# Kernel optimization log

Hardware: AMD Instinct MI355X
Metric: run time of the kernel (lower is better)

## Reference

```python
import jax, jax.numpy as jnp
import numpy as np

T_IN, A_IN, V_IN = 300, 74, 36
T_H, A_H, V_H = 256, 64, 64
ATTN_IN = 2 * (T_H + A_H + V_H)   # 768
MEM = 256
NN1 = NN2 = G1D = G2D = 512
OUT_IN = T_H + A_H + V_H + MEM    # 640
OUT_H, OUT_D = 512, 1
T_STEPS, N = 128, 512


def setup_inputs() -> dict:
    key = jax.random.key(0)
    ks = iter(jax.random.split(key, 64))

    def w(shape):
        return (jax.random.normal(next(ks), shape, jnp.float32) * 0.05)

    inp = {
        "x_p": jax.random.normal(next(ks), (T_STEPS, N, T_IN + A_IN + V_IN), jnp.float32),
        "c_t": jnp.zeros((N, T_H), jnp.float32),
        "c_a": jnp.zeros((N, A_H), jnp.float32),
        "c_v": jnp.zeros((N, V_H), jnp.float32),
        "mem": jnp.zeros((N, MEM), jnp.float32),
        # LSTMCell params (PyTorch layout: W_ih [4H, in], W_hh [4H, H], fused bias)
        "t_Wi": w((4 * T_H, T_IN)), "t_Wh": w((4 * T_H, T_H)), "t_b": w((4 * T_H,)),
        "a_Wi": w((4 * A_H, A_IN)), "a_Wh": w((4 * A_H, A_H)), "a_b": w((4 * A_H,)),
        "v_Wi": w((4 * V_H, V_IN)), "v_Wh": w((4 * V_H, V_H)), "v_b": w((4 * V_H,)),
        # attention / gating MLPs (PyTorch Linear layout: [out, in])
        "attn1_w1": w((NN1, ATTN_IN)), "attn1_b1": w((NN1,)),
        "attn1_w2": w((ATTN_IN, NN1)), "attn1_b2": w((ATTN_IN,)),
        "attn2_w1": w((NN2, ATTN_IN)), "attn2_b1": w((NN2,)),
        "attn2_w2": w((MEM, NN2)), "attn2_b2": w((MEM,)),
        "g1_w1": w((G1D, ATTN_IN + MEM)), "g1_b1": w((G1D,)),
        "g1_w2": w((MEM, G1D)), "g1_b2": w((MEM,)),
        "g2_w1": w((G2D, ATTN_IN + MEM)), "g2_b1": w((G2D,)),
        "g2_w2": w((MEM, G2D)), "g2_b2": w((MEM,)),
        "out_w1": w((OUT_H, OUT_IN)), "out_b1": w((OUT_H,)),
        "out_w2": w((OUT_D, OUT_H)), "out_b2": w((OUT_D,)),
    }
    return inp


def _lstm_cell(x, h, c, Wi, Wh, b):
    # PyTorch LSTMCell: gates ordered i, f, g, o
    z = x @ Wi.T + h @ Wh.T + b
    i, f, g, o = jnp.split(z, 4, axis=1)
    c2 = jax.nn.sigmoid(f) * c + jax.nn.sigmoid(i) * jnp.tanh(g)
    h2 = jax.nn.sigmoid(o) * jnp.tanh(c2)
    return h2, c2


def _mlp2(x, w1, b1, w2, b2):
    return jax.nn.relu(x @ w1.T + b1) @ w2.T + b2


def reference(x_p, c_t, c_a, c_v, mem,
              t_Wi, t_Wh, t_b, a_Wi, a_Wh, a_b, v_Wi, v_Wh, v_b,
              attn1_w1, attn1_b1, attn1_w2, attn1_b2,
              attn2_w1, attn2_b1, attn2_w2, attn2_b2,
              g1_w1, g1_b1, g1_w2, g1_b2,
              g2_w1, g2_b1, g2_w2, g2_b2,
              out_w1, out_b1, out_w2, out_b2):
    n = x_p.shape[1]
    init = (jnp.zeros((n, T_H), x_p.dtype), c_t,
            jnp.zeros((n, A_H), x_p.dtype), c_a,
            jnp.zeros((n, V_H), x_p.dtype), c_v,
            mem)

    def step(carry, x):
        th, tc, ah, ac, vh, vc, m = carry
        xt = x[:, :T_IN]
        xa = x[:, T_IN:T_IN + A_IN]
        xv = x[:, T_IN + A_IN:]
        pre_c = jnp.concatenate([tc, ac, vc], axis=1)
        th2, tc2 = _lstm_cell(xt, th, tc, t_Wi, t_Wh, t_b)
        ah2, ac2 = _lstm_cell(xa, ah, ac, a_Wi, a_Wh, a_b)
        vh2, vc2 = _lstm_cell(xv, vh, vc, v_Wi, v_Wh, v_b)
        cur_c = jnp.concatenate([tc2, ac2, vc2], axis=1)
        c_star = jnp.concatenate([pre_c, cur_c], axis=1)          # [n, 768]
        attention = jax.nn.softmax(_mlp2(c_star, attn1_w1, attn1_b1, attn1_w2, attn1_b2), axis=1)
        attended = attention * c_star
        c_hat = jnp.tanh(_mlp2(attended, attn2_w1, attn2_b1, attn2_w2, attn2_b2))
        both = jnp.concatenate([attended, m], axis=1)             # [n, 1024]
        gamma1 = jax.nn.sigmoid(_mlp2(both, g1_w1, g1_b1, g1_w2, g1_b2))
        gamma2 = jax.nn.sigmoid(_mlp2(both, g2_w1, g2_b1, g2_w2, g2_b2))
        m2 = gamma1 * m + gamma2 * c_hat
        return (th2, tc2, ah2, ac2, vh2, vc2, m2), None

    (th, tc, ah, ac, vh, vc, m), _ = jax.lax.scan(step, init, x_p)
    last_h = jnp.concatenate([th, ah, vh, m], axis=1)             # [n, 640]
    return _mlp2(last_h, out_w1, out_b1, out_w2, out_b2)          # [n, 1]
```

## Files before the change

kernel.cpp:

```cpp
#include <hip/hip_runtime.h>
#include <hip/hip_bf16.h>
#include <hip/hip_fp16.h>

typedef unsigned int u32;
typedef unsigned long long u64;
typedef __fp16 h2t __attribute__((ext_vector_type(2)));

#define T_STEPS_D 128
#define NBATCH 512

#define OFF_TWI   0L
#define OFF_AWI   284672L
#define OFF_VWI   302592L
#define OFF_A1W1  315392L
#define OFF_A1W2  512000L
#define OFF_A2W1  708608L
#define OFF_A2W2  905216L
#define OFF_GW1   970752L
#define OFF_GW2   1495040L
#define OFF_OW1   1626112L
#define U32_TOTAL 1789952L
#define FLAGS_OFF 1791744L
#define ATTQ_OFF  1792000L
#define OWP_OFF   2578432L
#define ATOMIC_RLX_AG(p, v) __hip_atomic_store((p), (v), __ATOMIC_RELAXED, __HIP_MEMORY_SCOPE_AGENT)
#define ATOMIC_LD_AG(p)     __hip_atomic_load((p), __ATOMIC_RELAXED, __HIP_MEMORY_SCOPE_AGENT)

__device__ __forceinline__ float sigm(float x) { return 1.f / (1.f + __expf(-x)); }
__device__ __forceinline__ float tanh_fast(float x) {
    float e = __expf(2.f * x);
    return 1.f - 2.f / (e + 1.f);
}
__device__ __forceinline__ float dot2(u32 a, u32 b, float c) {
    union { u32 u; h2t h; } x, y; x.u = a; y.u = b;
#if __has_builtin(__builtin_amdgcn_fdot2)
    return __builtin_amdgcn_fdot2(x.h, y.h, c, false);
#else
    c += (float)x.h[0] * (float)y.h[0];
    c += (float)x.h[1] * (float)y.h[1];
    return c;
#endif
}
__device__ __forceinline__ u32 pk2(float a, float b) {
    union { h2t h; u32 u; } z;
    z.h = __builtin_amdgcn_cvt_pkrtz(a, b);
    return z.u;
}

__device__ __forceinline__ void gp_load1(u32* buf, const u32* __restrict__ wp, int N) {
#pragma unroll
    for (int q = 0; q < 4; ++q) {
        uint2 v = *(const uint2*)(wp + q * 2 * N);
        buf[2 * q] = v.x; buf[2 * q + 1] = v.y;
    }
}
__device__ __forceinline__ void gp_load2(u32* buf, const u32* __restrict__ wp, int N) {
#pragma unroll
    for (int q = 0; q < 4; ++q) {
        uint4 v = *(const uint4*)(wp + q * 2 * N);
        buf[4 * q] = v.x; buf[4 * q + 1] = v.y; buf[4 * q + 2] = v.z; buf[4 * q + 3] = v.w;
    }
}

template<int NC>
__device__ __forceinline__ void gp_comp(float* acc, const u32* __restrict__ a, int stA,
                                        int kb, const u32* buf) {
#pragma unroll
    for (int r = 0; r < 4; ++r) {
        uint4 xa = *(const uint4*)(a + r * stA + kb);
        uint4 xb = *(const uint4*)(a + r * stA + kb + 4);
        u32 av[8] = {xa.x, xa.y, xa.z, xa.w, xb.x, xb.y, xb.z, xb.w};
#pragma unroll
        for (int p = 0; p < 8; ++p) {
            if constexpr (NC == 1) {
                acc[r] = dot2(buf[p], av[p], acc[r]);
            } else {
                acc[2 * r]     = dot2(buf[4 * (p >> 1) + (p & 1)],     av[p], acc[2 * r]);
                acc[2 * r + 1] = dot2(buf[4 * (p >> 1) + 2 + (p & 1)], av[p], acc[2 * r + 1]);
            }
        }
    }
}

template<int NC, int DEPTH>
__device__ __forceinline__ void gpart(float* acc, const u32* __restrict__ a, int k2, int stA,
                                      const u32* __restrict__ w, int N)
{
    const int nb = k2 >> 3;
    u32 b0[NC * 8], b1[NC * 8], b2[NC * 8];
#define GLOAD(B, P) do { if constexpr (NC == 1) gp_load1(B, w + (long)(P) * 8 * N, N); \
                         else gp_load2(B, w + (long)(P) * 8 * N, N); } while (0)
    if (nb > 0) GLOAD(b0, 0);
    if (DEPTH > 1 && nb > 1) GLOAD(b1, 1);
    if (DEPTH > 2 && nb > 2) GLOAD(b2, 2);
    int i = 0;
    while (i < nb) {
        gp_comp<NC>(acc, a, stA, i * 8, b0);
        if (i + DEPTH < nb) GLOAD(b0, i + DEPTH);
        ++i; if (i >= nb) break;
        gp_comp<NC>(acc, a, stA, i * 8, b1);
        if (i + DEPTH < nb) GLOAD(b1, i + DEPTH);
        ++i; if (i >= nb) break;
        if (DEPTH > 2) {
            gp_comp<NC>(acc, a, stA, i * 8, b2);
            if (i + DEPTH < nb) GLOAD(b2, i + DEPTH);
            ++i;
        }
    }
#undef GLOAD
    for (int p = nb * 8; p < k2; ++p) {
        const u32* wp = w + (long)(p >> 1) * 2 * N + (p & 1);
#pragma unroll
        for (int r = 0; r < 4; ++r) {
            u32 aa = a[r * stA + p];
            if constexpr (NC == 1) {
                acc[r] = dot2(wp[0], aa, acc[r]);
            } else {
                acc[2 * r]     = dot2(wp[0], aa, acc[2 * r]);
                acc[2 * r + 1] = dot2(wp[2], aa, acc[2 * r + 1]);
            }
        }
    }
}

__global__ void k_transpose(const float* __restrict__ src, unsigned short* __restrict__ dst,
                            int N, int K, int strideU, int rowOffK, int colOff)
{
    long i = (long)blockIdx.x * 256 + threadIdx.x;
    if (i >= (long)N * K) return;
    int n = (int)(i / K);
    int k = (int)(i - (long)n * K);
    __half h = __float2half(src[i]);
    long kk = k + rowOffK;
    long idx32 = (kk >> 2) * 2L * strideU + 2L * (colOff + n) + ((kk >> 1) & 1);
    dst[idx32 * 2 + (kk & 1)] = __half_as_ushort(h);
}

__global__ void k_packbias(const float* __restrict__ g1b1, const float* __restrict__ g2b1,
                           const float* __restrict__ g1b2, const float* __restrict__ g2b2,
                           float* __restrict__ gb)
{
    int i = blockIdx.x * 256 + threadIdx.x;
    if (i < 512) gb[i] = g1b1[i];
    else if (i < 1024) gb[i] = g2b1[i - 512];
    else if (i < 1280) gb[i] = g1b2[i - 1024];
    else if (i < 1536) gb[i] = g2b2[i - 1280];
}

__global__ __launch_bounds__(512)
void fused_rnn(const float* __restrict__ x_p,
               const float* __restrict__ c_t0, const float* __restrict__ c_a0,
               const float* __restrict__ c_v0, const float* __restrict__ mem0,
               const float* __restrict__ t_b, const float* __restrict__ a_b,
               const float* __restrict__ v_b,
               const float* __restrict__ a1b1, const float* __restrict__ a1b2,
               const float* __restrict__ a2b1, const float* __restrict__ a2b2,
               const float* __restrict__ ob1, const float* __restrict__ ow2,
               const float* __restrict__ ob2,
               const u32* __restrict__ wsu, const float* __restrict__ wsf,
               u32* wsrw,
               float* __restrict__ out)
{
    const int tid = threadIdx.x;
    const int xcd = (int)blockIdx.x & 7;
    const bool isA = xcd < 4;
    const int g = ((int)blockIdx.x >> 3) * 4 + (xcd & 3);
    const int row0 = g * 4;

    int* flagA = (int*)(wsrw + FLAGS_OFF);
    int* flagB = flagA + 128;
    u32* attq = wsrw + ATTQ_OFF;
    u32* owp = wsrw + OWP_OFF;

    __shared__ alignas(16) float sZ[4][1024];
    __shared__ alignas(16) float sZa[4][256];
    __shared__ alignas(16) float sZv[4][256];
    __shared__ alignas(16) float sTc[4][256];
    __shared__ alignas(16) float sAc[4][64];
    __shared__ alignas(16) float sVc[4][64];
    __shared__ alignas(16) float sM[4][256];
    __shared__ alignas(16) float sCs[4][768];
    __shared__ alignas(16) float sCp[2][4][256];
    __shared__ alignas(16) float sHid[4][512];
    __shared__ alignas(16) float sPart[2][4][512];
    __shared__ alignas(16) u32 pX[4][212];
    __shared__ alignas(16) u32 pCs[4][384];
    __shared__ alignas(16) u32 pTh[4][128];
    __shared__ alignas(16) u32 pAh[4][32];
    __shared__ alignas(16) u32 pVh[4][32];
    __shared__ alignas(16) u32 pM[4][128];
    __shared__ alignas(16) u32 pHid[4][256];
    __shared__ alignas(16) u32 pZ[4][512];
    __shared__ float sRed[4];
    __shared__ float sRed2[8][4];

    if (isA) {
        for (int i = tid; i < 4 * 128; i += 512) {
            int r = i >> 7, j2 = i & 127, j = 2 * j2;
            sTc[r][j] = c_t0[(row0 + r) * 256 + j];
            sTc[r][j + 1] = c_t0[(row0 + r) * 256 + j + 1];
            pTh[r][j2] = 0u;
        }
        for (int i = tid; i < 4 * 32; i += 512) {
            int r = i >> 5, j2 = i & 31, j = 2 * j2;
            sAc[r][j] = c_a0[(row0 + r) * 64 + j]; sAc[r][j + 1] = c_a0[(row0 + r) * 64 + j + 1];
            sVc[r][j] = c_v0[(row0 + r) * 64 + j]; sVc[r][j + 1] = c_v0[(row0 + r) * 64 + j + 1];
            pAh[r][j2] = 0u; pVh[r][j2] = 0u;
        }
        if (tid < 12) pX[tid / 3][189 + tid % 3] = 0u;
        __syncthreads();

        for (int t = 0; t < T_STEPS_D; ++t) {
            if (t >= 4) {
                if (tid == 0) {
                    while (__hip_atomic_load(flagB + g, __ATOMIC_ACQUIRE,
                                             __HIP_MEMORY_SCOPE_AGENT) < t - 3)
                        __builtin_amdgcn_s_sleep(2);
                }
                __syncthreads();
            }
            const float* xb = x_p + ((long)t * NBATCH + row0) * 410;
            for (int i = tid; i < 4 * 205; i += 512) {
                int r = i / 205, p = i - r * 205;
                float2 v = *(const float2*)(xb + r * 410 + 2 * p);
                int dst = (p < 150) ? p : (p < 187 ? p + 2 : p + 5);
                pX[r][dst] = pk2(v.x, v.y);
            }
            for (int i = tid; i < 4 * 192; i += 512) {
                int r = i / 192, p = i - r * 192;
                float v0, v1; int c;
                if (p < 128) { c = 2 * p; v0 = sTc[r][c]; v1 = sTc[r][c + 1]; }
                else if (p < 160) { int j = 2 * (p - 128); c = 256 + j; v0 = sAc[r][j]; v1 = sAc[r][j + 1]; }
                else { int j = 2 * (p - 160); c = 320 + j; v0 = sVc[r][j]; v1 = sVc[r][j + 1]; }
                sCs[r][c] = v0; sCs[r][c + 1] = v1;
                pCs[r][p] = pk2(v0, v1);
            }
            __syncthreads();

            {
                float acc[8] = {0.f, 0.f, 0.f, 0.f, 0.f, 0.f, 0.f, 0.f};
                gpart<2, 2>(acc, &pX[0][0], 150, 212, wsu + OFF_TWI + 4 * tid, 1024);
                gpart<2, 2>(acc, &pTh[0][0], 128, 128, wsu + OFF_TWI + 150L * 1024 + 4 * tid, 1024);
                float bb0 = t_b[2 * tid], bb1 = t_b[2 * tid + 1];
#pragma unroll
                for (int r = 0; r < 4; ++r) {
                    sZ[r][2 * tid] = acc[2 * r] + bb0;
                    sZ[r][2 * tid + 1] = acc[2 * r + 1] + bb1;
                }
            }
            if (tid < 256) {
                float acc[4] = {0.f, 0.f, 0.f, 0.f};
                gpart<1, 3>(acc, &pX[0][152], 38, 212, wsu + OFF_AWI + 2 * tid, 256);
                gpart<1, 3>(acc, &pAh[0][0], 32, 32, wsu + OFF_AWI + 38L * 256 + 2 * tid, 256);
                float b = a_b[tid];
#pragma unroll
                for (int r = 0; r < 4; ++r) sZa[r][tid] = acc[r] + b;
            } else {
                int st = tid - 256;
                float acc[4] = {0.f, 0.f, 0.f, 0.f};
                gpart<1, 3>(acc, &pX[0][192], 18, 212, wsu + OFF_VWI + 2 * st, 256);
                gpart<1, 3>(acc, &pVh[0][0], 32, 32, wsu + OFF_VWI + 18L * 256 + 2 * st, 256);
                float b = v_b[st];
#pragma unroll
                for (int r = 0; r < 4; ++r) sZv[r][st] = acc[r] + b;
            }
            __syncthreads();

            {
                int j = tid & 255;
                for (int r = tid >> 8; r < 4; r += 2) {
                    float iv = sZ[r][j], fv = sZ[r][256 + j], gv = sZ[r][512 + j], ov = sZ[r][768 + j];
                    float c2 = sigm(fv) * sTc[r][j] + sigm(iv) * tanh_fast(gv);
                    float h2 = sigm(ov) * tanh_fast(c2);
                    sTc[r][j] = c2; sCs[r][384 + j] = c2;
                    float c2o = __shfl_xor(c2, 1), h2o = __shfl_xor(h2, 1);
                    if (!(j & 1)) {
                        pTh[r][j >> 1] = pk2(h2, h2o);
                        pCs[r][192 + (j >> 1)] = pk2(c2, c2o);
                    }
                }
                int cell = tid >> 8, r2 = (tid >> 6) & 3, j2 = tid & 63;
                if (cell == 0) {
                    float iv = sZa[r2][j2], fv = sZa[r2][64 + j2], gv = sZa[r2][128 + j2], ov = sZa[r2][192 + j2];
                    float c2 = sigm(fv) * sAc[r2][j2] + sigm(iv) * tanh_fast(gv);
                    float h2 = sigm(ov) * tanh_fast(c2);
                    sAc[r2][j2] = c2; sCs[r2][640 + j2] = c2;
                    float c2o = __shfl_xor(c2, 1), h2o = __shfl_xor(h2, 1);
                    if (!(j2 & 1)) {
                        pAh[r2][j2 >> 1] = pk2(h2, h2o);
                        pCs[r2][320 + (j2 >> 1)] = pk2(c2, c2o);
                    }
                } else {
                    float iv = sZv[r2][j2], fv = sZv[r2][64 + j2], gv = sZv[r2][128 + j2], ov = sZv[r2][192 + j2];
                    float c2 = sigm(fv) * sVc[r2][j2] + sigm(iv) * tanh_fast(gv);
                    float h2 = sigm(ov) * tanh_fast(c2);
                    sVc[r2][j2] = c2; sCs[r2][704 + j2] = c2;
                    float c2o = __shfl_xor(c2, 1), h2o = __shfl_xor(h2, 1);
                    if (!(j2 & 1)) {
                        pVh[r2][j2 >> 1] = pk2(h2, h2o);
                        pCs[r2][352 + (j2 >> 1)] = pk2(c2, c2o);
                    }
                }
            }
            __syncthreads();

            {
                int half = tid >> 8, st = tid & 255;
                float acc[8] = {0.f, 0.f, 0.f, 0.f, 0.f, 0.f, 0.f, 0.f};
                gpart<2, 2>(acc, &pCs[0][half * 192], 192, 384,
                            wsu + OFF_A1W1 + (long)half * 192 * 512 + 4 * st, 512);
#pragma unroll
                for (int r = 0; r < 4; ++r) {
                    sPart[half][r][2 * st] = acc[2 * r];
                    sPart[half][r][2 * st + 1] = acc[2 * r + 1];
                }
            }
            __syncthreads();
            for (int i = tid; i < 1024; i += 512) {
                int r = i >> 8, cp = i & 255, c = 2 * cp;
                float v0 = fmaxf(sPart[0][r][c] + sPart[1][r][c] + a1b1[c], 0.f);
                float v1 = fmaxf(sPart[0][r][c + 1] + sPart[1][r][c + 1] + a1b1[c + 1], 0.f);
                pHid[r][cp] = pk2(v0, v1);
            }
            __syncthreads();

            if (tid < 384) {
                float acc[8] = {0.f, 0.f, 0.f, 0.f, 0.f, 0.f, 0.f, 0.f};
                gpart<2, 2>(acc, &pHid[0][0], 256, 256, wsu + OFF_A1W2 + 4 * tid, 768);
                float bb0 = a1b2[2 * tid], bb1 = a1b2[2 * tid + 1];
#pragma unroll
                for (int r = 0; r < 4; ++r) {
                    sZ[r][2 * tid] = acc[2 * r] + bb0;
                    sZ[r][2 * tid + 1] = acc[2 * r + 1] + bb1;
                }
            }
            __syncthreads();

            {
                int wv = tid >> 6, ln = tid & 63;
                if (wv < 4) {
                    float mx = -3.0e38f;
                    for (int i = ln; i < 768; i += 64) mx = fmaxf(mx, sZ[wv][i]);
                    for (int o = 32; o; o >>= 1) mx = fmaxf(mx, __shfl_xor(mx, o));
                    float sum = 0.f;
                    for (int i = ln; i < 768; i += 64) { float e = __expf(sZ[wv][i] - mx); sZ[wv][i] = e; sum += e; }
                    for (int o = 32; o; o >>= 1) sum += __shfl_xor(sum, o);
                    if (ln == 0) sRed[wv] = 1.f / sum;
                }
            }
            __syncthreads();
            {
                u64* dst = (u64*)(attq + ((long)(t & 3) * NBATCH + row0) * 384);
                for (int ii = tid; ii < 768; ii += 512) {
                    int base = 2 * ii;
                    int r = base / 384, p = base - r * 384, c = 2 * p;
                    float s = sRed[r];
                    u32 w0 = pk2(sZ[r][c] * s * sCs[r][c], sZ[r][c + 1] * s * sCs[r][c + 1]);
                    u32 w1 = pk2(sZ[r][c + 2] * s * sCs[r][c + 2], sZ[r][c + 3] * s * sCs[r][c + 3]);
                    ATOMIC_RLX_AG(dst + ii, (u64)w0 | ((u64)w1 << 32));
                }
            }
            __syncthreads();
            if (tid == 0)
                __hip_atomic_store(flagA + g, t + 1, __ATOMIC_RELEASE, __HIP_MEMORY_SCOPE_AGENT);
        }

        {
            float acc[4] = {0.f, 0.f, 0.f, 0.f};
            gpart<1, 3>(acc, &pTh[0][0], 128, 128, wsu + OFF_OW1 + 2 * tid, 512);
            gpart<1, 3>(acc, &pAh[0][0], 32, 32, wsu + OFF_OW1 + 128L * 512 + 2 * tid, 512);
            gpart<1, 3>(acc, &pVh[0][0], 32, 32, wsu + OFF_OW1 + 160L * 512 + 2 * tid, 512);
#pragma unroll
            for (int r = 0; r < 4; ++r)
                ATOMIC_RLX_AG(owp + (long)(row0 + r) * 512 + tid, __float_as_uint(acc[r]));
        }
        __syncthreads();
        if (tid == 0)
            __hip_atomic_store(flagA + g, 1000, __ATOMIC_RELEASE, __HIP_MEMORY_SCOPE_AGENT);

    } else {
        for (int i = tid; i < 4 * 128; i += 512) {
            int r = i >> 7, j2 = i & 127, j = 2 * j2;
            float m0 = mem0[(row0 + r) * 256 + j], m1 = mem0[(row0 + r) * 256 + j + 1];
            sM[r][j] = m0; sM[r][j + 1] = m1;
            pM[r][j2] = pk2(m0, m1);
        }
        __syncthreads();

        for (int t = 0; t < T_STEPS_D; ++t) {
            if (tid == 0) {
                while (__hip_atomic_load(flagA + g, __ATOMIC_ACQUIRE,
                                         __HIP_MEMORY_SCOPE_AGENT) < t + 1)
                    __builtin_amdgcn_s_sleep(2);
            }
            __syncthreads();
            {
                const u64* src = (const u64*)(attq + ((long)(t & 3) * NBATCH + row0) * 384);
                for (int ii = tid; ii < 768; ii += 512) {
                    u64 v = ATOMIC_LD_AG(src + ii);
                    int base = 2 * ii, r = base / 384, p = base - r * 384;
                    pCs[r][p] = (u32)v;
                    pCs[r][p + 1] = (u32)(v >> 32);
                }
            }
            __syncthreads();
            if (tid == 0)
                __hip_atomic_store(flagB + g, t + 1, __ATOMIC_RELEASE, __HIP_MEMORY_SCOPE_AGENT);

            {
                int half = tid >> 8, st = tid & 255;
                float acc[8] = {0.f, 0.f, 0.f, 0.f, 0.f, 0.f, 0.f, 0.f};
                gpart<2, 2>(acc, &pCs[0][half * 192], 192, 384,
                            wsu + OFF_A2W1 + (long)half * 192 * 512 + 4 * st, 512);
#pragma unroll
                for (int r = 0; r < 4; ++r) {
                    sPart[half][r][2 * st] = acc[2 * r];
                    sPart[half][r][2 * st + 1] = acc[2 * r + 1];
                }
            }
            {
                float acc[8] = {0.f, 0.f, 0.f, 0.f, 0.f, 0.f, 0.f, 0.f};
                gpart<2, 2>(acc, &pCs[0][0], 384, 384, wsu + OFF_GW1 + 4 * tid, 1024);
                gpart<2, 2>(acc, &pM[0][0], 128, 128, wsu + OFF_GW1 + 384L * 1024 + 4 * tid, 1024);
                float bb0 = wsf[2 * tid], bb1 = wsf[2 * tid + 1];
#pragma unroll
                for (int r = 0; r < 4; ++r) {
                    float v0 = fmaxf(acc[2 * r] + bb0, 0.f);
                    float v1 = fmaxf(acc[2 * r + 1] + bb1, 0.f);
                    pZ[r][tid] = pk2(v0, v1);
                }
            }
            __syncthreads();
            for (int i = tid; i < 1024; i += 512) {
                int r = i >> 8, cp = i & 255, c = 2 * cp;
                float v0 = fmaxf(sPart[0][r][c] + sPart[1][r][c] + a2b1[c], 0.f);
                float v1 = fmaxf(sPart[0][r][c + 1] + sPart[1][r][c + 1] + a2b1[c + 1], 0.f);
                pHid[r][cp] = pk2(v0, v1);
            }
            __syncthreads();

            {
                int half = tid >> 8, st = tid & 255;
                float acc[8] = {0.f, 0.f, 0.f, 0.f, 0.f, 0.f, 0.f, 0.f};
                const u32* actb = &pZ[0][(st >= 128 ? 256 : 0) + half * 128];
                gpart<2, 2>(acc, actb, 128, 512,
                            wsu + OFF_GW2 + (long)half * 128 * 512 + 4 * st, 512);
#pragma unroll
                for (int r = 0; r < 4; ++r) {
                    sPart[half][r][2 * st] = acc[2 * r];
                    sPart[half][r][2 * st + 1] = acc[2 * r + 1];
                }
            }
            {
                int kh = tid >> 8, col = tid & 255;
                float acc[4] = {0.f, 0.f, 0.f, 0.f};
                gpart<1, 3>(acc, &pHid[0][kh * 128], 128, 256,
                            wsu + OFF_A2W2 + (long)kh * 128 * 256 + 2 * col, 256);
#pragma unroll
                for (int r = 0; r < 4; ++r) sCp[kh][r][col] = acc[r];
            }
            __syncthreads();

            {
                int j = tid & 255;
                for (int r = tid >> 8; r < 4; r += 2) {
                    float g1raw = sPart[0][r][j] + sPart[1][r][j] + wsf[1024 + j];
                    float g2raw = sPart[0][r][256 + j] + sPart[1][r][256 + j] + wsf[1280 + j];
                    float g1v = sigm(g1raw);
                    float g2v = sigm(g2raw);
                    float ch = tanh_fast(sCp[0][r][j] + sCp[1][r][j] + a2b2[j]);
                    float m2 = g1v * sM[r][j] + g2v * ch;
                    sM[r][j] = m2;
                    float m2o = __shfl_xor(m2, 1);
                    if (!(j & 1)) pM[r][j >> 1] = pk2(m2, m2o);
                }
            }
            __syncthreads();
        }

        {
            float acc[4] = {0.f, 0.f, 0.f, 0.f};
            gpart<1, 3>(acc, &pM[0][0], 128, 128, wsu + OFF_OW1 + 192L * 512 + 2 * tid, 512);
            if (tid == 0) {
                while (__hip_atomic_load(flagA + g, __ATOMIC_ACQUIRE,
                                         __HIP_MEMORY_SCOPE_AGENT) < 1000)
                    __builtin_amdgcn_s_sleep(2);
            }
            __syncthreads();
            float wv2 = ow2[tid], b = ob1[tid];
            float pr[4];
#pragma unroll
            for (int r = 0; r < 4; ++r) {
                float ap = __uint_as_float(ATOMIC_LD_AG(owp + (long)(row0 + r) * 512 + tid));
                float h = fmaxf(acc[r] + ap + b, 0.f);
                pr[r] = h * wv2;
            }
#pragma unroll
            for (int o = 32; o; o >>= 1) {
#pragma unroll
                for (int r = 0; r < 4; ++r) pr[r] += __shfl_xor(pr[r], o);
            }
            int wvid = tid >> 6, ln = tid & 63;
            if (ln == 0) {
#pragma unroll
                for (int r = 0; r < 4; ++r) sRed2[wvid][r] = pr[r];
            }
            __syncthreads();
            if (tid < 4) {
                float s = 0.f;
#pragma unroll
                for (int w = 0; w < 8; ++w) s += sRed2[w][tid];
                out[row0 + tid] = s + ob2[0];
            }
        }
    }
}

extern "C" void kernel_launch(void* const* d_in, const int* in_sizes, int n_in,
                              void* d_out, int out_size, void* d_ws, size_t ws_size,
                              hipStream_t stream)
{
    const float* x_p  = (const float*)d_in[0];
    const float* c_t  = (const float*)d_in[1];
    const float* c_a  = (const float*)d_in[2];
    const float* c_v  = (const float*)d_in[3];
    const float* memp = (const float*)d_in[4];

    u32* wsu = (u32*)d_ws;
    float* wsf = (float*)((char*)d_ws + (size_t)U32_TOTAL * 4);

    hipMemsetAsync((char*)d_ws + (size_t)OFF_AWI * 4, 0, (size_t)(OFF_VWI - OFF_AWI) * 4, stream);
    hipMemsetAsync((char*)d_ws + (size_t)FLAGS_OFF * 4, 0, 1024, stream);

    auto T = [&](const void* src, long off, int N, int K, int strideU, int rowOffK, int colOff) {
        long total = (long)N * K;
        int blocks = (int)((total + 255) / 256);
        hipLaunchKernelGGL(k_transpose, dim3(blocks), dim3(256), 0, stream,
                           (const float*)src, (unsigned short*)(wsu + off), N, K, strideU, rowOffK, colOff);
    };
    T(d_in[5],  OFF_TWI,  1024, 300, 1024, 0,   0);
    T(d_in[6],  OFF_TWI,  1024, 256, 1024, 300, 0);
    T(d_in[8],  OFF_AWI,  256,  74,  256,  0,   0);
    T(d_in[9],  OFF_AWI,  256,  64,  256,  76,  0);
    T(d_in[11], OFF_VWI,  256,  36,  256,  0,   0);
    T(d_in[12], OFF_VWI,  256,  64,  256,  36,  0);
    T(d_in[14], OFF_A1W1, 512,  768, 512,  0,   0);
    T(d_in[16], OFF_A1W2, 768,  512, 768,  0,   0);
    T(d_in[18], OFF_A2W1, 512,  768, 512,  0,   0);
    T(d_in[20], OFF_A2W2, 256,  512, 256,  0,   0);
    T(d_in[22], OFF_GW1,  512, 1024, 1024, 0,   0);
    T(d_in[26], OFF_GW1,  512, 1024, 1024, 0,   512);
    T(d_in[24], OFF_GW2,  256,  512, 512,  0,   0);
    T(d_in[28], OFF_GW2,  256,  512, 512,  0,   256);
    T(d_in[30], OFF_OW1,  512,  640, 512,  0,   0);

    hipLaunchKernelGGL(k_packbias, dim3(6), dim3(256), 0, stream,
                       (const float*)d_in[23], (const float*)d_in[27],
                       (const float*)d_in[25], (const float*)d_in[29], wsf);

    hipLaunchKernelGGL(fused_rnn, dim3(256), dim3(512), 0, stream,
                       x_p, c_t, c_a, c_v, memp,
                       (const float*)d_in[7],  (const float*)d_in[10], (const float*)d_in[13],
                       (const float*)d_in[15], (const float*)d_in[17],
                       (const float*)d_in[19], (const float*)d_in[21],
                       (const float*)d_in[31], (const float*)d_in[32], (const float*)d_in[33],
                       wsu, wsf, wsu, (float*)d_out);
}
```

Baseline: 8.856 ms.

## Move half of attn2 first-layer GEMV to producer blocks via global queue

Producer (A) blocks now compute the attn2 layer-1 partial product over the first half of the attended vector (the pre_c part) and publish it through a new ring buffer in global memory. Consumer (B) blocks read this partial and compute only the second half, which rebalances work across the two block groups of the pipeline. The change also raises a gpart template parameter from 2 to 3 in several places and adds a minimum-blocks hint of 2 to the launch bounds. It adds extra global traffic and a block-wide barrier on the producer side, and the occupancy hint may cause register spills.

```diff
diff --git a/kernel.cpp b/kernel.cpp
--- a/kernel.cpp
+++ b/kernel.cpp
@@ -23,6 +23,7 @@
 #define FLAGS_OFF 1791744L
 #define ATTQ_OFF  1792000L
 #define OWP_OFF   2578432L
+#define APQ_OFF   2840576L
 #define ATOMIC_RLX_AG(p, v) __hip_atomic_store((p), (v), __ATOMIC_RELAXED, __HIP_MEMORY_SCOPE_AGENT)
 #define ATOMIC_LD_AG(p)     __hip_atomic_load((p), __ATOMIC_RELAXED, __HIP_MEMORY_SCOPE_AGENT)
 
@@ -147,7 +148,7 @@
     else if (i < 1536) gb[i] = g2b2[i - 1280];
 }
 
-__global__ __launch_bounds__(512)
+__global__ __launch_bounds__(512, 2)
 void fused_rnn(const float* __restrict__ x_p,
                const float* __restrict__ c_t0, const float* __restrict__ c_a0,
                const float* __restrict__ c_v0, const float* __restrict__ mem0,
@@ -171,6 +172,7 @@
     int* flagB = flagA + 128;
     u32* attq = wsrw + ATTQ_OFF;
     u32* owp = wsrw + OWP_OFF;
+    u64* apq = (u64*)(wsrw + APQ_OFF);
 
     __shared__ alignas(16) float sZ[4][1024];
     __shared__ alignas(16) float sZa[4][256];
@@ -239,8 +241,8 @@
 
             {
                 float acc[8] = {0.f, 0.f, 0.f, 0.f, 0.f, 0.f, 0.f, 0.f};
-                gpart<2, 2>(acc, &pX[0][0], 150, 212, wsu + OFF_TWI + 4 * tid, 1024);
-                gpart<2, 2>(acc, &pTh[0][0], 128, 128, wsu + OFF_TWI + 150L * 1024 + 4 * tid, 1024);
+                gpart<2, 3>(acc, &pX[0][0], 150, 212, wsu + OFF_TWI + 4 * tid, 1024);
+                gpart<2, 3>(acc, &pTh[0][0], 128, 128, wsu + OFF_TWI + 150L * 1024 + 4 * tid, 1024);
                 float bb0 = t_b[2 * tid], bb1 = t_b[2 * tid + 1];
 #pragma unroll
                 for (int r = 0; r < 4; ++r) {
@@ -307,7 +309,7 @@
             {
                 int half = tid >> 8, st = tid & 255;
                 float acc[8] = {0.f, 0.f, 0.f, 0.f, 0.f, 0.f, 0.f, 0.f};
-                gpart<2, 2>(acc, &pCs[0][half * 192], 192, 384,
+                gpart<2, 3>(acc, &pCs[0][half * 192], 192, 384,
                             wsu + OFF_A1W1 + (long)half * 192 * 512 + 4 * st, 512);
 #pragma unroll
                 for (int r = 0; r < 4; ++r) {
@@ -326,7 +328,7 @@
 
             if (tid < 384) {
                 float acc[8] = {0.f, 0.f, 0.f, 0.f, 0.f, 0.f, 0.f, 0.f};
-                gpart<2, 2>(acc, &pHid[0][0], 256, 256, wsu + OFF_A1W2 + 4 * tid, 768);
+                gpart<2, 3>(acc, &pHid[0][0], 256, 256, wsu + OFF_A1W2 + 4 * tid, 768);
                 float bb0 = a1b2[2 * tid], bb1 = a1b2[2 * tid + 1];
 #pragma unroll
                 for (int r = 0; r < 4; ++r) {
@@ -357,7 +359,23 @@
                     float s = sRed[r];
                     u32 w0 = pk2(sZ[r][c] * s * sCs[r][c], sZ[r][c + 1] * s * sCs[r][c + 1]);
                     u32 w1 = pk2(sZ[r][c + 2] * s * sCs[r][c + 2], sZ[r][c + 3] * s * sCs[r][c + 3]);
+                    pCs[r][p] = w0; pCs[r][p + 1] = w1;
                     ATOMIC_RLX_AG(dst + ii, (u64)w0 | ((u64)w1 << 32));
+                }
+            }
+            __syncthreads();
+
+            {
+                float acc[4] = {0.f, 0.f, 0.f, 0.f};
+                gpart<1, 3>(acc, &pCs[0][0], 192, 384, wsu + OFF_A2W1 + 2 * tid, 512);
+                u64* dst = apq + ((long)(t & 3) * NBATCH + row0) * 256;
+#pragma unroll
+                for (int r = 0; r < 4; ++r) {
+                    float f1 = __shfl_xor(acc[r], 1);
+                    if (!(tid & 1)) {
+                        u64 v = (u64)__float_as_uint(acc[r]) | ((u64)__float_as_uint(f1) << 32);
+                        ATOMIC_RLX_AG(dst + r * 256 + (tid >> 1), v);
+                    }
                 }
             }
             __syncthreads();
@@ -402,26 +420,29 @@
                     pCs[r][p] = (u32)v;
                     pCs[r][p + 1] = (u32)(v >> 32);
                 }
+                const u64* src2 = apq + ((long)(t & 3) * NBATCH + row0) * 256;
+                for (int ii = tid; ii < 1024; ii += 512) {
+                    u64 v = ATOMIC_LD_AG(src2 + ii);
+                    int r = ii >> 8, cp = ii & 255;
+                    sPart[1][r][2 * cp] = __uint_as_float((u32)v);
+                    sPart[1][r][2 * cp + 1] = __uint_as_float((u32)(v >> 32));
+                }
             }
             __syncthreads();
             if (tid == 0)
                 __hip_atomic_store(flagB + g, t + 1, __ATOMIC_RELEASE, __HIP_MEMORY_SCOPE_AGENT);
 
             {
-                int half = tid >> 8, st = tid & 255;
+                float acc[4] = {0.f, 0.f, 0.f, 0.f};
+                gpart<1, 3>(acc, &pCs[0][192], 192, 384,
+                            wsu + OFF_A2W1 + 192L * 512 + 2 * tid, 512);
+#pragma unroll
+                for (int r = 0; r < 4; ++r) sPart[0][r][tid] = acc[r];
+            }
+            {
                 float acc[8] = {0.f, 0.f, 0.f, 0.f, 0.f, 0.f, 0.f, 0.f};
-                gpart<2, 2>(acc, &pCs[0][half * 192], 192, 384,
-                            wsu + OFF_A2W1 + (long)half * 192 * 512 + 4 * st, 512);
-#pragma unroll
-                for (int r = 0; r < 4; ++r) {
-                    sPart[half][r][2 * st] = acc[2 * r];
-                    sPart[half][r][2 * st + 1] = acc[2 * r + 1];
-                }
-            }
-            {
-                float acc[8] = {0.f, 0.f, 0.f, 0.f, 0.f, 0.f, 0.f, 0.f};
-                gpart<2, 2>(acc, &pCs[0][0], 384, 384, wsu + OFF_GW1 + 4 * tid, 1024);
-                gpart<2, 2>(acc, &pM[0][0], 128, 128, wsu + OFF_GW1 + 384L * 1024 + 4 * tid, 1024);
+                gpart<2, 3>(acc, &pCs[0][0], 384, 384, wsu + OFF_GW1 + 4 * tid, 1024);
+                gpart<2, 3>(acc, &pM[0][0], 128, 128, wsu + OFF_GW1 + 384L * 1024 + 4 * tid, 1024);
                 float bb0 = wsf[2 * tid], bb1 = wsf[2 * tid + 1];
 #pragma unroll
                 for (int r = 0; r < 4; ++r) {
@@ -433,8 +454,8 @@
             __syncthreads();
             for (int i = tid; i < 1024; i += 512) {
                 int r = i >> 8, cp = i & 255, c = 2 * cp;
-                float v0 = fmaxf(sPart[0][r][c] + sPart[1][r][c] + a2b1[c], 0.f);
-                float v1 = fmaxf(sPart[0][r][c + 1] + sPart[1][r][c + 1] + a2b1[c + 1], 0.f);
+                float v0 = fmaxf(sPart[1][r][c] + sPart[0][r][c] + a2b1[c], 0.f);
+                float v1 = fmaxf(sPart[1][r][c + 1] + sPart[0][r][c + 1] + a2b1[c + 1], 0.f);
                 pHid[r][cp] = pk2(v0, v1);
             }
             __syncthreads();
@@ -443,7 +464,7 @@
                 int half = tid >> 8, st = tid & 255;
                 float acc[8] = {0.f, 0.f, 0.f, 0.f, 0.f, 0.f, 0.f, 0.f};
                 const u32* actb = &pZ[0][(st >= 128 ? 256 : 0) + half * 128];
-                gpart<2, 2>(acc, actb, 128, 512,
+                gpart<2, 3>(acc, actb, 128, 512,
                             wsu + OFF_GW2 + (long)half * 128 * 512 + 4 * st, 512);
 #pragma unroll
                 for (int r = 0; r < 4; ++r) {
```

Measured after the change: 28.67 ms. 224% more time.
